# Performance work log

Hardware: AMD Instinct MI355X
Metric: run time of the kernel (lower is better)

Reference implementation:

```python
import jax, jax.numpy as jnp
import numpy as np

DIN_OBJ = 128
DIN_PRED = 128
H = 512
DOUT = 128
NUM_OBJS = 50000
NUM_TRIPLES = 200000


def _kaiming(key, fan_in, fan_out):
    # kaiming_normal_ default: std = sqrt(2 / fan_in)
    return jax.random.normal(key, (fan_in, fan_out), dtype=jnp.float32) * np.sqrt(2.0 / fan_in)


def setup_inputs() -> dict:
    key = jax.random.key(0)
    ks = jax.random.split(key, 8)
    obj_vecs = jax.random.normal(ks[0], (NUM_OBJS, DIN_OBJ), dtype=jnp.float32)
    pred_vecs = jax.random.normal(ks[1], (NUM_TRIPLES, DIN_PRED), dtype=jnp.float32)
    edges = jax.random.randint(ks[2], (NUM_TRIPLES, 2), 0, NUM_OBJS, dtype=jnp.int64)
    # net1: [2*Din_obj + Din_pred, H, 2*H + Dout], ReLU after each linear
    W1a = _kaiming(ks[3], 2 * DIN_OBJ + DIN_PRED, H)
    b1a = jnp.zeros((H,), jnp.float32)
    W1b = _kaiming(ks[4], H, 2 * H + DOUT)
    b1b = jnp.zeros((2 * H + DOUT,), jnp.float32)
    # net2: [H, H, Dout]
    W2a = _kaiming(ks[5], H, H)
    b2a = jnp.zeros((H,), jnp.float32)
    W2b = _kaiming(ks[6], H, DOUT)
    b2b = jnp.zeros((DOUT,), jnp.float32)
    return {"obj_vecs": obj_vecs, "pred_vecs": pred_vecs, "edges": edges,
            "W1a": W1a, "b1a": b1a, "W1b": W1b, "b1b": b1b,
            "W2a": W2a, "b2a": b2a, "W2b": W2b, "b2b": b2b}


def reference(obj_vecs, pred_vecs, edges, W1a, b1a, W1b, b1b, W2a, b2a, W2b, b2b):
    num_objs = obj_vecs.shape[0]
    num_triples = pred_vecs.shape[0]
    s_idx = edges[:, 0]
    o_idx = edges[:, 1]
    # gather subject/object vectors, concat with predicate vectors  [T, 2*Din_obj+Din_pred]
    cur_t = jnp.concatenate([obj_vecs[s_idx], pred_vecs, obj_vecs[o_idx]], axis=1)
    # net1: Linear-ReLU-Linear-ReLU
    h = jax.nn.relu(cur_t @ W1a + b1a)
    new_t = jax.nn.relu(h @ W1b + b1b)          # [T, 2H+Dout]
    new_s = new_t[:, :H]
    new_p = new_t[:, H:H + DOUT]
    new_o = new_t[:, H + DOUT:]
    # scatter-add pool onto objects  [N, H]
    pooled = jax.ops.segment_sum(new_s, s_idx, num_segments=num_objs)
    pooled = pooled + jax.ops.segment_sum(new_o, o_idx, num_segments=num_objs)
    # avg pooling: divide by per-object triple count (clamped to >= 1)
    ones = jnp.ones((num_triples,), obj_vecs.dtype)
    counts = jax.ops.segment_sum(ones, s_idx, num_segments=num_objs)
    counts = counts + jax.ops.segment_sum(ones, o_idx, num_segments=num_objs)
    counts = jnp.maximum(counts, 1.0)
    pooled = pooled / counts[:, None]
    # net2: Linear-ReLU-Linear-ReLU
    h2 = jax.nn.relu(pooled @ W2a + b2a)
    new_obj = jax.nn.relu(h2 @ W2b + b2b)       # [N, Dout]
    return new_obj, new_p
```

## Files before the change

### kernel.cpp

```cpp
#include <hip/hip_runtime.h>
#include <hip/hip_bf16.h>
#include <stdint.h>

typedef __bf16 bf16x8 __attribute__((ext_vector_type(8)));
typedef __bf16 bf16x4 __attribute__((ext_vector_type(4)));
typedef float  f32x4  __attribute__((ext_vector_type(4)));

#define DIN   128
#define KA    384
#define HD    512
#define NB    1152
#define DOUTD 128
#define NOBJ  50000
#define NTRI  200000
#define TM    64
#define NSCAN 98
#define SB_STRIDE 520

__global__ void detect_i64(const int* __restrict__ e, int* __restrict__ flag) {
    int i = blockIdx.x * 256 + threadIdx.x;
    if (i < NTRI && e[2 * i + 1] != 0) atomicOr(flag, 1);
}
__global__ void normalize_edges(const int* __restrict__ e, const int* __restrict__ flag,
                                int* __restrict__ sidx, int* __restrict__ oidx) {
    int t = blockIdx.x * 256 + threadIdx.x;
    if (t >= NTRI) return;
    bool is64 = (*flag == 0);
    int s = is64 ? e[4 * t]     : e[2 * t];
    int o = is64 ? e[4 * t + 2] : e[2 * t + 1];
    s = s < 0 ? 0 : (s >= NOBJ ? NOBJ - 1 : s);
    o = o < 0 ? 0 : (o >= NOBJ ? NOBJ - 1 : o);
    sidx[t] = s; oidx[t] = o;
}

__global__ void pack_w(const float* __restrict__ W, __bf16* __restrict__ P, int K, int N) {
    int idx = blockIdx.x * 256 + threadIdx.x;
    int total = (K / 32) * (N / 16) * 64;
    if (idx >= total) return;
    int lane = idx & 63;
    int f    = idx >> 6;
    int NT   = N / 16;
    int kt = f / NT, nt = f - kt * NT;
    int krow = kt * 32 + (lane >> 4) * 8;
    int col  = nt * 16 + (lane & 15);
    __bf16 tmp[8];
#pragma unroll
    for (int i = 0; i < 8; i++) tmp[i] = (__bf16)W[(size_t)(krow + i) * N + col];
    *reinterpret_cast<bf16x8*>(P + (size_t)idx * 8) = *reinterpret_cast<const bf16x8*>(tmp);
}

__global__ void count_int(const int* __restrict__ sidx, const int* __restrict__ oidx,
                          int* __restrict__ cnt) {
    int t = blockIdx.x * 256 + threadIdx.x;
    if (t >= NTRI) return;
    atomicAdd(&cnt[sidx[t]], 1);
    atomicAdd(&cnt[oidx[t]], 1);
}

__global__ void scanA(const int* __restrict__ cnt, int* __restrict__ sums) {
    __shared__ int sh[512];
    int idx = blockIdx.x * 512 + threadIdx.x;
    sh[threadIdx.x] = idx < NOBJ ? cnt[idx] : 0;
    __syncthreads();
    for (int s = 256; s > 0; s >>= 1) {
        if (threadIdx.x < s) sh[threadIdx.x] += sh[threadIdx.x + s];
        __syncthreads();
    }
    if (threadIdx.x == 0) sums[blockIdx.x] = sh[0];
}
__global__ void scanB(int* __restrict__ sums) {
    if (threadIdx.x == 0) {
        int run = 0;
        for (int i = 0; i < NSCAN; i++) { int v = sums[i]; sums[i] = run; run += v; }
    }
}
__global__ void scanC(const int* __restrict__ cnt, const int* __restrict__ sums,
                      int* __restrict__ offs, int* __restrict__ cursor) {
    __shared__ int sh[512];
    int idx = blockIdx.x * 512 + threadIdx.x;
    int v = idx < NOBJ ? cnt[idx] : 0;
    sh[threadIdx.x] = v;
    __syncthreads();
    for (int d = 1; d < 512; d <<= 1) {
        int t = (threadIdx.x >= d) ? sh[threadIdx.x - d] : 0;
        __syncthreads();
        sh[threadIdx.x] += t;
        __syncthreads();
    }
    if (idx < NOBJ) {
        int excl = sh[threadIdx.x] - v + sums[blockIdx.x];
        offs[idx] = excl; cursor[idx] = excl;
    }
}
__global__ void fill_refs(const int* __restrict__ sidx, const int* __restrict__ oidx,
                          int* __restrict__ cursor, int* __restrict__ refs) {
    int t = blockIdx.x * 256 + threadIdx.x;
    if (t >= NTRI) return;
    int p = atomicAdd(&cursor[sidx[t]], 1); refs[p] = 2 * t;
    int q = atomicAdd(&cursor[oidx[t]], 1); refs[q] = 2 * t + 1;
}

__global__ __launch_bounds__(512) void pool_mean(
    const __bf16* __restrict__ newso, const int* __restrict__ cnt,
    const int* __restrict__ offs, const int* __restrict__ refs,
    __bf16* __restrict__ xbuf)
{
    int w    = (blockIdx.x * 512 + threadIdx.x) >> 6;
    int lane = threadIdx.x & 63;
    if (w >= NOBJ) return;
    int n = cnt[w], off = offs[w];
    float acc[8];
#pragma unroll
    for (int i = 0; i < 8; i++) acc[i] = 0.f;
    for (int j = 0; j < n; j++) {
        int r = refs[off + j];
        const __bf16* src = newso + (size_t)(r >> 1) * 1024 + (r & 1) * 512 + lane * 8;
        bf16x8 v = *reinterpret_cast<const bf16x8*>(src);
#pragma unroll
        for (int i = 0; i < 8; i++) acc[i] += (float)v[i];
    }
    float inv = 1.f / (n > 0 ? (float)n : 1.f);
    bf16x8 o;
#pragma unroll
    for (int i = 0; i < 8; i++) o[i] = (__bf16)(acc[i] * inv);
    *reinterpret_cast<bf16x8*>(xbuf + (size_t)w * 512 + lane * 8) = o;
}

__global__ __launch_bounds__(512, 4) void fused12(
    const float* __restrict__ obj, const float* __restrict__ pred,
    const int* __restrict__ sidx, const int* __restrict__ oidx,
    const __bf16* __restrict__ pW1a, const float* __restrict__ b1a,
    const __bf16* __restrict__ pW1b, const float* __restrict__ b1b,
    float* __restrict__ out_p, __bf16* __restrict__ newso)
{
    extern __shared__ char smem[];
    __bf16* sB = (__bf16*)smem;

    const int tid  = threadIdx.x;
    const int lane = tid & 63;
    const int wn   = tid >> 6;
    const int t0   = blockIdx.x * TM;

    const int lk    = (lane >> 4) * 8;
    const int lr    = lane & 15;
    const int rbase = (lane >> 4) * 4;

    for (int u = tid; u < 64 * 96; u += 512) {
        int part = u & 31;
        int seg  = (u >> 5) % 3;
        int row  = u / 96;
        int t    = t0 + row;
        const float* src;
        if (seg == 0)      src = obj  + (size_t)sidx[t] * DIN;
        else if (seg == 1) src = pred + (size_t)t       * DIN;
        else               src = obj  + (size_t)oidx[t] * DIN;
        float4 v = *reinterpret_cast<const float4*>(src + part * 4);
        bf16x4 w;
        w[0] = (__bf16)v.x; w[1] = (__bf16)v.y; w[2] = (__bf16)v.z; w[3] = (__bf16)v.w;
        *reinterpret_cast<bf16x4*>(sB + row * SB_STRIDE + seg * 128 + part * 4) = w;
    }
    __syncthreads();

    {
        f32x4 acc[4][4];
#pragma unroll
        for (int mi = 0; mi < 4; mi++)
#pragma unroll
            for (int ni = 0; ni < 4; ni++) acc[mi][ni] = (f32x4){0.f, 0.f, 0.f, 0.f};

        bf16x8 bc[4];
#pragma unroll
        for (int ni = 0; ni < 4; ni++)
            bc[ni] = *reinterpret_cast<const bf16x8*>(pW1a + (((size_t)(wn * 4 + ni)) * 64 + lane) * 8);

        for (int kt = 0; kt < KA / 32; ++kt) {
            int ktn = (kt + 1 < KA / 32) ? kt + 1 : kt;
            bf16x8 bn[4];
#pragma unroll
            for (int ni = 0; ni < 4; ni++)
                bn[ni] = *reinterpret_cast<const bf16x8*>(pW1a + (((size_t)(ktn * 32 + wn * 4 + ni)) * 64 + lane) * 8);

            bf16x8 a[4];
#pragma unroll
            for (int mi = 0; mi < 4; mi++)
                a[mi] = *reinterpret_cast<const bf16x8*>(sB + (mi * 16 + lr) * SB_STRIDE + kt * 32 + lk);

#pragma unroll
            for (int ni = 0; ni < 4; ni++)
#pragma unroll
                for (int mi = 0; mi < 4; mi++)
                    acc[mi][ni] = __builtin_amdgcn_mfma_f32_16x16x32_bf16(a[mi], bc[ni], acc[mi][ni], 0, 0, 0);

#pragma unroll
            for (int ni = 0; ni < 4; ni++) bc[ni] = bn[ni];
        }
        __syncthreads();

#pragma unroll
        for (int ni = 0; ni < 4; ni++) {
            int col = wn * 64 + ni * 16 + lr;
            float bv = b1a[col];
#pragma unroll
            for (int mi = 0; mi < 4; mi++)
#pragma unroll
                for (int r = 0; r < 4; r++) {
                    float v = acc[mi][ni][r] + bv;
                    v = v > 0.f ? v : 0.f;
                    sB[(mi * 16 + rbase + r) * SB_STRIDE + col] = (__bf16)v;
                }
        }
    }
    __syncthreads();

    for (int pp = 0; pp < 3; ++pp) {
        f32x4 acc2[4][3];
#pragma unroll
        for (int mi = 0; mi < 4; mi++)
#pragma unroll
            for (int ni = 0; ni < 3; ni++) acc2[mi][ni] = (f32x4){0.f, 0.f, 0.f, 0.f};

        bf16x8 bc[3];
#pragma unroll
        for (int ni = 0; ni < 3; ni++)
            bc[ni] = *reinterpret_cast<const bf16x8*>(pW1b + (((size_t)(wn * 9 + pp * 3 + ni)) * 64 + lane) * 8);

        for (int kt = 0; kt < HD / 32; ++kt) {
            int ktn = (kt + 1 < HD / 32) ? kt + 1 : kt;
            bf16x8 bn[3];
#pragma unroll
            for (int ni = 0; ni < 3; ni++)
                bn[ni] = *reinterpret_cast<const bf16x8*>(pW1b + (((size_t)(ktn * 72 + wn * 9 + pp * 3 + ni)) * 64 + lane) * 8);

            bf16x8 a[4];
#pragma unroll
            for (int mi = 0; mi < 4; mi++)
                a[mi] = *reinterpret_cast<const bf16x8*>(sB + (mi * 16 + lr) * SB_STRIDE + kt * 32 + lk);

#pragma unroll
            for (int ni = 0; ni < 3; ni++)
#pragma unroll
                for (int mi = 0; mi < 4; mi++)
                    acc2[mi][ni] = __builtin_amdgcn_mfma_f32_16x16x32_bf16(a[mi], bc[ni], acc2[mi][ni], 0, 0, 0);

#pragma unroll
            for (int ni = 0; ni < 3; ni++) bc[ni] = bn[ni];
        }
#pragma unroll
        for (int ni = 0; ni < 3; ni++) {
            int c = wn * 144 + pp * 48 + ni * 16 + lr;
            float bv = b1b[c];
#pragma unroll
            for (int mi = 0; mi < 4; mi++)
#pragma unroll
                for (int r = 0; r < 4; r++) {
                    int row = mi * 16 + rbase + r;
                    int t   = t0 + row;
                    float v = acc2[mi][ni][r] + bv;
                    v = v > 0.f ? v : 0.f;
                    if (c < HD) {
                        newso[(size_t)t * 1024 + c] = (__bf16)v;
                    } else if (c < HD + DOUTD) {
                        out_p[(size_t)t * DOUTD + (c - HD)] = v;
                    } else {
                        newso[(size_t)t * 1024 + 512 + (c - HD - DOUTD)] = (__bf16)v;
                    }
                }
        }
    }
}

__global__ __launch_bounds__(512, 4) void fused34(
    const __bf16* __restrict__ xbuf,
    const __bf16* __restrict__ pW2a, const float* __restrict__ b2a,
    const __bf16* __restrict__ pW2b, const float* __restrict__ b2b,
    float* __restrict__ out_obj)
{
    extern __shared__ char smem[];
    __bf16* sX = (__bf16*)smem;

    const int tid  = threadIdx.x;
    const int lane = tid & 63;
    const int wid  = tid >> 6;
    const int o0   = blockIdx.x * TM;

    for (int u = tid; u < 64 * 64; u += 512) {
        int part = u & 63;
        int row  = u >> 6;
        int ob   = o0 + row;
        bf16x8 v;
        if (ob < NOBJ) v = *reinterpret_cast<const bf16x8*>(xbuf + (size_t)ob * 512 + part * 8);
        else { bf16x8 z = {}; v = z; }
        *reinterpret_cast<bf16x8*>(sX + row * SB_STRIDE + part * 8) = v;
    }
    __syncthreads();

    const int wm = wid >> 2;
    const int wn = wid & 3;
    const int lk = (lane >> 4) * 8;
    const int lr = lane & 15;
    const int rbase = (lane >> 4) * 4;

    {
        f32x4 acc[2][8];
#pragma unroll
        for (int mi = 0; mi < 2; mi++)
#pragma unroll
            for (int ni = 0; ni < 8; ni++) acc[mi][ni] = (f32x4){0.f, 0.f, 0.f, 0.f};

        bf16x8 bc[8];
#pragma unroll
        for (int ni = 0; ni < 8; ni++)
            bc[ni] = *reinterpret_cast<const bf16x8*>(pW2a + (((size_t)(wn * 8 + ni)) * 64 + lane) * 8);

        for (int kt = 0; kt < HD / 32; ++kt) {
            int ktn = (kt + 1 < HD / 32) ? kt + 1 : kt;
            bf16x8 bn[8];
#pragma unroll
            for (int ni = 0; ni < 8; ni++)
                bn[ni] = *reinterpret_cast<const bf16x8*>(pW2a + (((size_t)(ktn * 32 + wn * 8 + ni)) * 64 + lane) * 8);

            bf16x8 a0 = *reinterpret_cast<const bf16x8*>(sX + (wm * 32 + lr) * SB_STRIDE + kt * 32 + lk);
            bf16x8 a1 = *reinterpret_cast<const bf16x8*>(sX + (wm * 32 + 16 + lr) * SB_STRIDE + kt * 32 + lk);
#pragma unroll
            for (int ni = 0; ni < 8; ni++) {
                acc[0][ni] = __builtin_amdgcn_mfma_f32_16x16x32_bf16(a0, bc[ni], acc[0][ni], 0, 0, 0);
                acc[1][ni] = __builtin_amdgcn_mfma_f32_16x16x32_bf16(a1, bc[ni], acc[1][ni], 0, 0, 0);
            }
#pragma unroll
            for (int ni = 0; ni < 8; ni++) bc[ni] = bn[ni];
        }
        __syncthreads();

#pragma unroll
        for (int mi = 0; mi < 2; mi++)
#pragma unroll
            for (int ni = 0; ni < 8; ni++) {
                int col = wn * 128 + ni * 16 + lr;
                float bv = b2a[col];
#pragma unroll
                for (int r = 0; r < 4; r++) {
                    float v = acc[mi][ni][r] + bv;
                    v = v > 0.f ? v : 0.f;
                    sX[(wm * 32 + mi * 16 + rbase + r) * SB_STRIDE + col] = (__bf16)v;
                }
            }
    }
    __syncthreads();

    {
        f32x4 acc[2][2];
#pragma unroll
        for (int mi = 0; mi < 2; mi++)
#pragma unroll
            for (int ni = 0; ni < 2; ni++) acc[mi][ni] = (f32x4){0.f, 0.f, 0.f, 0.f};

        for (int kt = 0; kt < HD / 32; ++kt) {
            bf16x8 a0 = *reinterpret_cast<const bf16x8*>(sX + (wm * 32 + lr) * SB_STRIDE + kt * 32 + lk);
            bf16x8 a1 = *reinterpret_cast<const bf16x8*>(sX + (wm * 32 + 16 + lr) * SB_STRIDE + kt * 32 + lk);
#pragma unroll
            for (int ni = 0; ni < 2; ni++) {
                int f = kt * 8 + wn * 2 + ni;
                bf16x8 b = *reinterpret_cast<const bf16x8*>(pW2b + ((size_t)f * 64 + lane) * 8);
                acc[0][ni] = __builtin_amdgcn_mfma_f32_16x16x32_bf16(a0, b, acc[0][ni], 0, 0, 0);
                acc[1][ni] = __builtin_amdgcn_mfma_f32_16x16x32_bf16(a1, b, acc[1][ni], 0, 0, 0);
            }
        }
#pragma unroll
        for (int mi = 0; mi < 2; mi++)
#pragma unroll
            for (int ni = 0; ni < 2; ni++) {
                int col = wn * 32 + ni * 16 + lr;
                float bv = b2b[col];
#pragma unroll
                for (int r = 0; r < 4; r++) {
                    int row = wm * 32 + mi * 16 + rbase + r;
                    int ob  = o0 + row;
                    if (ob < NOBJ) {
                        float v = acc[mi][ni][r] + bv;
                        v = v > 0.f ? v : 0.f;
                        out_obj[(size_t)ob * DOUTD + col] = v;
                    }
                }
            }
    }
}

extern "C" void kernel_launch(void* const* d_in, const int* in_sizes, int n_in,
                              void* d_out, int out_size, void* d_ws, size_t ws_size,
                              hipStream_t stream)
{
    const float* obj   = (const float*)d_in[0];
    const float* pred  = (const float*)d_in[1];
    const int*   edges = (const int*)d_in[2];
    const float* W1a = (const float*)d_in[3];
    const float* b1a = (const float*)d_in[4];
    const float* W1b = (const float*)d_in[5];
    const float* b1b = (const float*)d_in[6];
    const float* W2a = (const float*)d_in[7];
    const float* b2a = (const float*)d_in[8];
    const float* W2b = (const float*)d_in[9];
    const float* b2b = (const float*)d_in[10];

    float* out_obj = (float*)d_out;
    float* out_p   = (float*)d_out + (size_t)NOBJ * DOUTD;

    char* ws = (char*)d_ws;
    int*    sidx   = (int*)ws;
    int*    oidx   = sidx + NTRI;
    int*    flag   = (int*)(ws + 1800000);
    __bf16* pW1a   = (__bf16*)(ws + 1800064);
    __bf16* pW1b   = pW1a + 196608;
    __bf16* pW2a   = pW1b + 589824;
    __bf16* pW2b   = pW2a + 262144;
    int*    cnt    = (int*)(ws + 4028416);
    int*    offs   = (int*)(ws + 4228416);
    int*    cursor = (int*)(ws + 4428416);
    int*    sums   = (int*)(ws + 4628416);
    int*    refs   = (int*)(ws + 4628928);
    __bf16* xbuf   = (__bf16*)(ws + 6228928);
    __bf16* newso  = (__bf16*)(ws + 57428928);

    hipMemsetAsync(flag, 0, 4, stream);
    detect_i64<<<(NTRI + 255) / 256, 256, 0, stream>>>(edges, flag);
    normalize_edges<<<(NTRI + 255) / 256, 256, 0, stream>>>(edges, flag, sidx, oidx);

    pack_w<<<(24576 + 255) / 256, 256, 0, stream>>>(W1a, pW1a, 384, 512);
    pack_w<<<(73728 + 255) / 256, 256, 0, stream>>>(W1b, pW1b, 512, 1152);
    pack_w<<<(32768 + 255) / 256, 256, 0, stream>>>(W2a, pW2a, 512, 512);
    pack_w<<<(8192  + 255) / 256, 256, 0, stream>>>(W2b, pW2b, 512, 128);

    hipMemsetAsync(cnt, 0, 200000, stream);
    count_int<<<(NTRI + 255) / 256, 256, 0, stream>>>(sidx, oidx, cnt);
    scanA<<<NSCAN, 512, 0, stream>>>(cnt, sums);
    scanB<<<1, 64, 0, stream>>>(sums);
    scanC<<<NSCAN, 512, 0, stream>>>(cnt, sums, offs, cursor);
    fill_refs<<<(NTRI + 255) / 256, 256, 0, stream>>>(sidx, oidx, cursor, refs);

    size_t lds12 = (size_t)64 * SB_STRIDE * 2;
    fused12<<<NTRI / TM, 512, lds12, stream>>>(obj, pred, sidx, oidx,
                                               pW1a, b1a, pW1b, b1b,
                                               out_p, newso);
    pool_mean<<<(NOBJ * 64 + 511) / 512, 512, 0, stream>>>(newso, cnt, offs, refs, xbuf);
    size_t lds34 = (size_t)64 * SB_STRIDE * 2;
    fused34<<<(NOBJ + TM - 1) / TM, 512, lds34, stream>>>(xbuf, pW2a, b2a, pW2b, b2b, out_obj);
}
```

Baseline: 1.031 ms.

## Split fused net1 into two tiled GEMMs with async global-to-LDS double buffering

When the workspace is large enough, the fused per-64-triple net1 kernel is replaced by bf16 pre-conversion of obj/pred, then two separate 128x128-tiled GEMM kernels. These use global_load_lds double buffering for both A (gathered rows) and B (packed weights), with the hidden activations written to an HBM buffer. This aims to improve weight reuse and MFMA utilisation over streaming weights per block, at the cost of extra HBM traffic for the bf16 copies and the 200000x512 hidden buffer. The legacy and net2 kernels also drop their register prefetch of weight fragments and load them inline instead.

```diff
diff --git a/kernel.cpp b/kernel.cpp
--- a/kernel.cpp
+++ b/kernel.cpp
@@ -13,9 +13,14 @@
 #define DOUTD 128
 #define NOBJ  50000
 #define NTRI  200000
-#define TM    64
 #define NSCAN 98
 #define SB_STRIDE 520
+
+__device__ __forceinline__ void gload16(const void* g, void* l) {
+    __builtin_amdgcn_global_load_lds(
+        (const __attribute__((address_space(1))) void*)g,
+        (__attribute__((address_space(3))) void*)l, 16, 0, 0);
+}
 
 __global__ void detect_i64(const int* __restrict__ e, int* __restrict__ flag) {
     int i = blockIdx.x * 256 + threadIdx.x;
@@ -31,6 +36,17 @@
     s = s < 0 ? 0 : (s >= NOBJ ? NOBJ - 1 : s);
     o = o < 0 ? 0 : (o >= NOBJ ? NOBJ - 1 : o);
     sidx[t] = s; oidx[t] = o;
+}
+
+__global__ void to_bf16(const float* __restrict__ in, __bf16* __restrict__ out, long n4) {
+    long i = (long)blockIdx.x * 256 + threadIdx.x;
+    long stride = (long)gridDim.x * 256;
+    for (; i < n4; i += stride) {
+        float4 v = reinterpret_cast<const float4*>(in)[i];
+        bf16x4 w;
+        w[0] = (__bf16)v.x; w[1] = (__bf16)v.y; w[2] = (__bf16)v.z; w[3] = (__bf16)v.w;
+        reinterpret_cast<bf16x4*>(out)[i] = w;
+    }
 }
 
 __global__ void pack_w(const float* __restrict__ W, __bf16* __restrict__ P, int K, int N) {
@@ -56,7 +72,6 @@
     atomicAdd(&cnt[sidx[t]], 1);
     atomicAdd(&cnt[oidx[t]], 1);
 }
-
 __global__ void scanA(const int* __restrict__ cnt, int* __restrict__ sums) {
     __shared__ int sh[512];
     int idx = blockIdx.x * 512 + threadIdx.x;
@@ -126,7 +141,179 @@
     *reinterpret_cast<bf16x8*>(xbuf + (size_t)w * 512 + lane * 8) = o;
 }
 
-__global__ __launch_bounds__(512, 4) void fused12(
+__global__ __launch_bounds__(256, 3) void gemm1(
+    const __bf16* __restrict__ objbf, const __bf16* __restrict__ predbf,
+    const int* __restrict__ sidx, const int* __restrict__ oidx,
+    const __bf16* __restrict__ pW1a, const float* __restrict__ b1a,
+    __bf16* __restrict__ hbuf)
+{
+    __shared__ char smem[32768];
+    char* sA = smem;
+    char* sB = smem + 16384;
+
+    const int tid = threadIdx.x, lane = tid & 63, wid = tid >> 6;
+    const int wm = wid >> 1, wn = wid & 1;
+    const int t0 = blockIdx.x * 128;
+    const int nb = blockIdx.y;
+
+    const int i0 = 2 * wid, i1 = i0 + 1;
+    int trA0 = t0 + i0 * 16 + (lane >> 2); if (trA0 >= NTRI) trA0 = NTRI - 1;
+    int trA1 = t0 + i1 * 16 + (lane >> 2); if (trA1 >= NTRI) trA1 = NTRI - 1;
+    const int cb0 = (lane & 3) * 16;
+    const char* srcS0 = (const char*)(objbf  + (size_t)sidx[trA0] * DIN) + cb0;
+    const char* srcP0 = (const char*)(predbf + (size_t)trA0 * DIN) + cb0;
+    const char* srcO0 = (const char*)(objbf  + (size_t)oidx[trA0] * DIN) + cb0;
+    const char* srcS1 = (const char*)(objbf  + (size_t)sidx[trA1] * DIN) + cb0;
+    const char* srcP1 = (const char*)(predbf + (size_t)trA1 * DIN) + cb0;
+    const char* srcO1 = (const char*)(objbf  + (size_t)oidx[trA1] * DIN) + cb0;
+    const char* pWc   = (const char*)pW1a + (size_t)lane * 16;
+
+    f32x4 acc[4][4];
+#pragma unroll
+    for (int mi = 0; mi < 4; mi++)
+#pragma unroll
+        for (int ni = 0; ni < 4; ni++) acc[mi][ni] = (f32x4){0.f, 0.f, 0.f, 0.f};
+
+    auto stage = [&](int buf, int kt) {
+        int third = kt >> 2;
+        int cb = (kt & 3) * 64;
+        const char* g0 = (third == 0 ? srcS0 : third == 1 ? srcP0 : srcO0) + cb;
+        const char* g1 = (third == 0 ? srcS1 : third == 1 ? srcP1 : srcO1) + cb;
+        gload16(g0, sA + buf * 8192 + i0 * 1024);
+        gload16(g1, sA + buf * 8192 + i1 * 1024);
+        const char* gb0 = pWc + (size_t)(kt * 32 + nb * 8 + i0) * 1024;
+        const char* gb1 = pWc + (size_t)(kt * 32 + nb * 8 + i1) * 1024;
+        gload16(gb0, sB + buf * 8192 + i0 * 1024);
+        gload16(gb1, sB + buf * 8192 + i1 * 1024);
+    };
+
+    int buf = 0;
+    stage(0, 0);
+    __syncthreads();
+    for (int kt = 0; kt < KA / 32; ++kt) {
+        if (kt + 1 < KA / 32) stage(buf ^ 1, kt + 1);
+        const char* aB = sA + buf * 8192;
+        const char* bB = sB + buf * 8192;
+        bf16x8 af[4], bf[4];
+#pragma unroll
+        for (int mi = 0; mi < 4; mi++) {
+            int row = wm * 64 + mi * 16 + (lane & 15);
+            af[mi] = *reinterpret_cast<const bf16x8*>(aB + row * 64 + (lane >> 4) * 16);
+        }
+#pragma unroll
+        for (int ni = 0; ni < 4; ni++)
+            bf[ni] = *reinterpret_cast<const bf16x8*>(bB + (wn * 4 + ni) * 1024 + lane * 16);
+#pragma unroll
+        for (int ni = 0; ni < 4; ni++)
+#pragma unroll
+            for (int mi = 0; mi < 4; mi++)
+                acc[mi][ni] = __builtin_amdgcn_mfma_f32_16x16x32_bf16(af[mi], bf[ni], acc[mi][ni], 0, 0, 0);
+        __syncthreads();
+        buf ^= 1;
+    }
+
+#pragma unroll
+    for (int ni = 0; ni < 4; ni++) {
+        int colg = nb * 128 + wn * 64 + ni * 16 + (lane & 15);
+        float bv = b1a[colg];
+#pragma unroll
+        for (int mi = 0; mi < 4; mi++)
+#pragma unroll
+            for (int r = 0; r < 4; r++) {
+                int trow = t0 + wm * 64 + mi * 16 + (lane >> 4) * 4 + r;
+                if (trow < NTRI) {
+                    float v = acc[mi][ni][r] + bv;
+                    v = v > 0.f ? v : 0.f;
+                    hbuf[(size_t)trow * HD + colg] = (__bf16)v;
+                }
+            }
+    }
+}
+
+__global__ __launch_bounds__(256, 3) void gemm2(
+    const __bf16* __restrict__ hbuf,
+    const __bf16* __restrict__ pW1b, const float* __restrict__ b1b,
+    float* __restrict__ out_p, __bf16* __restrict__ newso)
+{
+    __shared__ char smem[32768];
+    char* sA = smem;
+    char* sB = smem + 16384;
+
+    const int tid = threadIdx.x, lane = tid & 63, wid = tid >> 6;
+    const int wm = wid >> 1, wn = wid & 1;
+    const int t0 = blockIdx.x * 128;
+    const int nb = blockIdx.y;
+
+    const int i0 = 2 * wid, i1 = i0 + 1;
+    int trA0 = t0 + i0 * 16 + (lane >> 2); if (trA0 >= NTRI) trA0 = NTRI - 1;
+    int trA1 = t0 + i1 * 16 + (lane >> 2); if (trA1 >= NTRI) trA1 = NTRI - 1;
+    const int cb0 = (lane & 3) * 16;
+    const char* srcH0 = (const char*)(hbuf + (size_t)trA0 * HD) + cb0;
+    const char* srcH1 = (const char*)(hbuf + (size_t)trA1 * HD) + cb0;
+    const char* pWc   = (const char*)pW1b + (size_t)lane * 16;
+
+    f32x4 acc[4][4];
+#pragma unroll
+    for (int mi = 0; mi < 4; mi++)
+#pragma unroll
+        for (int ni = 0; ni < 4; ni++) acc[mi][ni] = (f32x4){0.f, 0.f, 0.f, 0.f};
+
+    auto stage = [&](int buf, int kt) {
+        int cb = kt * 64;
+        gload16(srcH0 + cb, sA + buf * 8192 + i0 * 1024);
+        gload16(srcH1 + cb, sA + buf * 8192 + i1 * 1024);
+        const char* gb0 = pWc + (size_t)(kt * 72 + nb * 8 + i0) * 1024;
+        const char* gb1 = pWc + (size_t)(kt * 72 + nb * 8 + i1) * 1024;
+        gload16(gb0, sB + buf * 8192 + i0 * 1024);
+        gload16(gb1, sB + buf * 8192 + i1 * 1024);
+    };
+
+    int buf = 0;
+    stage(0, 0);
+    __syncthreads();
+    for (int kt = 0; kt < HD / 32; ++kt) {
+        if (kt + 1 < HD / 32) stage(buf ^ 1, kt + 1);
+        const char* aB = sA + buf * 8192;
+        const char* bB = sB + buf * 8192;
+        bf16x8 af[4], bf[4];
+#pragma unroll
+        for (int mi = 0; mi < 4; mi++) {
+            int row = wm * 64 + mi * 16 + (lane & 15);
+            af[mi] = *reinterpret_cast<const bf16x8*>(aB + row * 64 + (lane >> 4) * 16);
+        }
+#pragma unroll
+        for (int ni = 0; ni < 4; ni++)
+            bf[ni] = *reinterpret_cast<const bf16x8*>(bB + (wn * 4 + ni) * 1024 + lane * 16);
+#pragma unroll
+        for (int ni = 0; ni < 4; ni++)
+#pragma unroll
+            for (int mi = 0; mi < 4; mi++)
+                acc[mi][ni] = __builtin_amdgcn_mfma_f32_16x16x32_bf16(af[mi], bf[ni], acc[mi][ni], 0, 0, 0);
+        __syncthreads();
+        buf ^= 1;
+    }
+
+#pragma unroll
+    for (int ni = 0; ni < 4; ni++) {
+        int colg = nb * 128 + wn * 64 + ni * 16 + (lane & 15);
+        float bv = b1b[colg];
+#pragma unroll
+        for (int mi = 0; mi < 4; mi++)
+#pragma unroll
+            for (int r = 0; r < 4; r++) {
+                int trow = t0 + wm * 64 + mi * 16 + (lane >> 4) * 4 + r;
+                if (trow < NTRI) {
+                    float v = acc[mi][ni][r] + bv;
+                    v = v > 0.f ? v : 0.f;
+                    if (nb < 4)       newso[(size_t)trow * 1024 + colg] = (__bf16)v;
+                    else if (nb == 4) out_p[(size_t)trow * DOUTD + (colg - HD)] = v;
+                    else              newso[(size_t)trow * 1024 + 512 + (colg - 640)] = (__bf16)v;
+                }
+            }
+    }
+}
+
+__global__ __launch_bounds__(512, 4) void fused12_legacy(
     const float* __restrict__ obj, const float* __restrict__ pred,
     const int* __restrict__ sidx, const int* __restrict__ oidx,
     const __bf16* __restrict__ pW1a, const float* __restrict__ b1a,
@@ -139,7 +326,7 @@
     const int tid  = threadIdx.x;
     const int lane = tid & 63;
     const int wn   = tid >> 6;
-    const int t0   = blockIdx.x * TM;
+    const int t0   = blockIdx.x * 64;
 
     const int lk    = (lane >> 4) * 8;
     const int lr    = lane & 15;
@@ -168,34 +355,20 @@
 #pragma unroll
             for (int ni = 0; ni < 4; ni++) acc[mi][ni] = (f32x4){0.f, 0.f, 0.f, 0.f};
 
-        bf16x8 bc[4];
-#pragma unroll
-        for (int ni = 0; ni < 4; ni++)
-            bc[ni] = *reinterpret_cast<const bf16x8*>(pW1a + (((size_t)(wn * 4 + ni)) * 64 + lane) * 8);
-
         for (int kt = 0; kt < KA / 32; ++kt) {
-            int ktn = (kt + 1 < KA / 32) ? kt + 1 : kt;
-            bf16x8 bn[4];
-#pragma unroll
-            for (int ni = 0; ni < 4; ni++)
-                bn[ni] = *reinterpret_cast<const bf16x8*>(pW1a + (((size_t)(ktn * 32 + wn * 4 + ni)) * 64 + lane) * 8);
-
             bf16x8 a[4];
 #pragma unroll
             for (int mi = 0; mi < 4; mi++)
                 a[mi] = *reinterpret_cast<const bf16x8*>(sB + (mi * 16 + lr) * SB_STRIDE + kt * 32 + lk);
-
-#pragma unroll
-            for (int ni = 0; ni < 4; ni++)
+#pragma unroll
+            for (int ni = 0; ni < 4; ni++) {
+                bf16x8 b = *reinterpret_cast<const bf16x8*>(pW1a + (((size_t)(kt * 32 + wn * 4 + ni)) * 64 + lane) * 8);
 #pragma unroll
                 for (int mi = 0; mi < 4; mi++)
-                    acc[mi][ni] = __builtin_amdgcn_mfma_f32_16x16x32_bf16(a[mi], bc[ni], acc[mi][ni], 0, 0, 0);
-
-#pragma unroll
-            for (int ni = 0; ni < 4; ni++) bc[ni] = bn[ni];
+                    acc[mi][ni] = __builtin_amdgcn_mfma_f32_16x16x32_bf16(a[mi], b, acc[mi][ni], 0, 0, 0);
+            }
         }
         __syncthreads();
-
 #pragma unroll
         for (int ni = 0; ni < 4; ni++) {
             int col = wn * 64 + ni * 16 + lr;
@@ -219,31 +392,18 @@
 #pragma unroll
             for (int ni = 0; ni < 3; ni++) acc2[mi][ni] = (f32x4){0.f, 0.f, 0.f, 0.f};
 
-        bf16x8 bc[3];
-#pragma unroll
-        for (int ni = 0; ni < 3; ni++)
-            bc[ni] = *reinterpret_cast<const bf16x8*>(pW1b + (((size_t)(wn * 9 + pp * 3 + ni)) * 64 + lane) * 8);
-
         for (int kt = 0; kt < HD / 32; ++kt) {
-            int ktn = (kt + 1 < HD / 32) ? kt + 1 : kt;
-            bf16x8 bn[3];
-#pragma unroll
-            for (int ni = 0; ni < 3; ni++)
-                bn[ni] = *reinterpret_cast<const bf16x8*>(pW1b + (((size_t)(ktn * 72 + wn * 9 + pp * 3 + ni)) * 64 + lane) * 8);
-
             bf16x8 a[4];
 #pragma unroll
             for (int mi = 0; mi < 4; mi++)
                 a[mi] = *reinterpret_cast<const bf16x8*>(sB + (mi * 16 + lr) * SB_STRIDE + kt * 32 + lk);
-
-#pragma unroll
-            for (int ni = 0; ni < 3; ni++)
+#pragma unroll
+            for (int ni = 0; ni < 3; ni++) {
+                bf16x8 b = *reinterpret_cast<const bf16x8*>(pW1b + (((size_t)(kt * 72 + wn * 9 + pp * 3 + ni)) * 64 + lane) * 8);
 #pragma unroll
                 for (int mi = 0; mi < 4; mi++)
-                    acc2[mi][ni] = __builtin_amdgcn_mfma_f32_16x16x32_bf16(a[mi], bc[ni], acc2[mi][ni], 0, 0, 0);
-
-#pragma unroll
-            for (int ni = 0; ni < 3; ni++) bc[ni] = bn[ni];
+                    acc2[mi][ni] = __builtin_amdgcn_mfma_f32_16x16x32_bf16(a[mi], b, acc2[mi][ni], 0, 0, 0);
+            }
         }
 #pragma unroll
         for (int ni = 0; ni < 3; ni++) {
@@ -257,13 +417,9 @@
                     int t   = t0 + row;
                     float v = acc2[mi][ni][r] + bv;
                     v = v > 0.f ? v : 0.f;
-                    if (c < HD) {
-                        newso[(size_t)t * 1024 + c] = (__bf16)v;
-                    } else if (c < HD + DOUTD) {
-                        out_p[(size_t)t * DOUTD + (c - HD)] = v;
-                    } else {
-                        newso[(size_t)t * 1024 + 512 + (c - HD - DOUTD)] = (__bf16)v;
-                    }
+                    if (c < HD) newso[(size_t)t * 1024 + c] = (__bf16)v;
+                    else if (c < HD + DOUTD) out_p[(size_t)t * DOUTD + (c - HD)] = v;
+                    else newso[(size_t)t * 1024 + 512 + (c - HD - DOUTD)] = (__bf16)v;
                 }
         }
     }
@@ -281,7 +437,7 @@
     const int tid  = threadIdx.x;
     const int lane = tid & 63;
     const int wid  = tid >> 6;
-    const int o0   = blockIdx.x * TM;
+    const int o0   = blockIdx.x * 64;
 
     for (int u = tid; u < 64 * 64; u += 512) {
         int part = u & 63;
@@ -307,27 +463,15 @@
 #pragma unroll
             for (int ni = 0; ni < 8; ni++) acc[mi][ni] = (f32x4){0.f, 0.f, 0.f, 0.f};
 
-        bf16x8 bc[8];
-#pragma unroll
-        for (int ni = 0; ni < 8; ni++)
-            bc[ni] = *reinterpret_cast<const bf16x8*>(pW2a + (((size_t)(wn * 8 + ni)) * 64 + lane) * 8);
-
         for (int kt = 0; kt < HD / 32; ++kt) {
-            int ktn = (kt + 1 < HD / 32) ? kt + 1 : kt;
-            bf16x8 bn[8];
-#pragma unroll
-            for (int ni = 0; ni < 8; ni++)
-                bn[ni] = *reinterpret_cast<const bf16x8*>(pW2a + (((size_t)(ktn * 32 + wn * 8 + ni)) * 64 + lane) * 8);
-
             bf16x8 a0 = *reinterpret_cast<const bf16x8*>(sX + (wm * 32 + lr) * SB_STRIDE + kt * 32 + lk);
             bf16x8 a1 = *reinterpret_cast<const bf16x8*>(sX + (wm * 32 + 16 + lr) * SB_STRIDE + kt * 32 + lk);
 #pragma unroll
             for (int ni = 0; ni < 8; ni++) {
-                acc[0][ni] = __builtin_amdgcn_mfma_f32_16x16x32_bf16(a0, bc[ni], acc[0][ni], 0, 0, 0);
-                acc[1][ni] = __builtin_amdgcn_mfma_f32_16x16x32_bf16(a1, bc[ni], acc[1][ni], 0, 0, 0);
-            }
-#pragma unroll
-            for (int ni = 0; ni < 8; ni++) bc[ni] = bn[ni];
+                bf16x8 b = *reinterpret_cast<const bf16x8*>(pW2a + (((size_t)(kt * 32 + wn * 8 + ni)) * 64 + lane) * 8);
+                acc[0][ni] = __builtin_amdgcn_mfma_f32_16x16x32_bf16(a0, b, acc[0][ni], 0, 0, 0);
+                acc[1][ni] = __builtin_amdgcn_mfma_f32_16x16x32_bf16(a1, b, acc[1][ni], 0, 0, 0);
+            }
         }
         __syncthreads();
 
@@ -419,6 +563,12 @@
     int*    refs   = (int*)(ws + 4628928);
     __bf16* xbuf   = (__bf16*)(ws + 6228928);
     __bf16* newso  = (__bf16*)(ws + 57428928);
+    __bf16* objbf  = (__bf16*)(ws + 467028928);
+    __bf16* predbf = (__bf16*)(ws + 479828928);
+    __bf16* hbuf   = (__bf16*)(ws + 531028928);
+    const size_t NEED_M97 = 735828928;
+
+    bool m97 = ws_size >= NEED_M97;
 
     hipMemsetAsync(flag, 0, 4, stream);
     detect_i64<<<(NTRI + 255) / 256, 256, 0, stream>>>(edges, flag);
@@ -436,11 +586,21 @@
     scanC<<<NSCAN, 512, 0, stream>>>(cnt, sums, offs, cursor);
     fill_refs<<<(NTRI + 255) / 256, 256, 0, stream>>>(sidx, oidx, cursor, refs);
 
-    size_t lds12 = (size_t)64 * SB_STRIDE * 2;
-    fused12<<<NTRI / TM, 512, lds12, stream>>>(obj, pred, sidx, oidx,
-                                               pW1a, b1a, pW1b, b1b,
-                                               out_p, newso);
+    if (m97) {
+        to_bf16<<<2048, 256, 0, stream>>>(obj,  objbf,  (long)NOBJ * DIN / 4);
+        to_bf16<<<2048, 256, 0, stream>>>(pred, predbf, (long)NTRI * DIN / 4);
+        dim3 g1((NTRI + 127) / 128, 4);
+        gemm1<<<g1, 256, 0, stream>>>(objbf, predbf, sidx, oidx, pW1a, b1a, hbuf);
+        dim3 g2((NTRI + 127) / 128, 9);
+        gemm2<<<g2, 256, 0, stream>>>(hbuf, pW1b, b1b, out_p, newso);
+    } else {
+        size_t lds12 = (size_t)64 * SB_STRIDE * 2;
+        fused12_legacy<<<NTRI / 64, 512, lds12, stream>>>(obj, pred, sidx, oidx,
+                                                          pW1a, b1a, pW1b, b1b,
+                                                          out_p, newso);
+    }
+
     pool_mean<<<(NOBJ * 64 + 511) / 512, 512, 0, stream>>>(newso, cnt, offs, refs, xbuf);
     size_t lds34 = (size_t)64 * SB_STRIDE * 2;
-    fused34<<<(NOBJ + TM - 1) / TM, 512, lds34, stream>>>(xbuf, pW2a, b2a, pW2b, b2b, out_obj);
-}
+    fused34<<<(NOBJ + 63) / 64, 512, lds34, stream>>>(xbuf, pW2a, b2a, pW2b, b2b, out_obj);
+}
```

New measurement: 1.047 ms. No clear change (+1.5%).
